# Optimization experiments

Measured on AMD Instinct MI355X. Metric: run time of the kernel, lower is better.

## Reference

```python
import jax, jax.numpy as jnp
from jax import lax
import numpy as np

NUM_TOKENS = 14
DIM = 512
B, T = 32, 512


def _lstm(xs, W_ih, W_hh, b_ih, b_hh):
    """PyTorch-semantics single-layer LSTM, batch_first. xs: [B,T,D] -> hs: [B,T,D].
    Gate order i, f, g, o; gates = x @ W_ih^T + b_ih + h @ W_hh^T + b_hh."""
    Bsz, Tlen, D = xs.shape
    # Precompute input contribution for all timesteps (one big GEMM).
    pre = jnp.einsum('btd,gd->btg', xs, W_ih) + (b_ih + b_hh)  # [B,T,4D]

    def step(carry, p):
        h, c = carry
        gates = p + h @ W_hh.T  # [B,4D]
        i, f, g, o = jnp.split(gates, 4, axis=-1)
        i = jax.nn.sigmoid(i)
        f = jax.nn.sigmoid(f)
        g = jnp.tanh(g)
        o = jax.nn.sigmoid(o)
        c = f * c + i * g
        h = o * jnp.tanh(c)
        return (h, c), h

    h0 = jnp.zeros((Bsz, D), xs.dtype)
    (_, _), hs = lax.scan(step, (h0, h0), jnp.swapaxes(pre, 0, 1))  # time-major scan
    return jnp.swapaxes(hs, 0, 1)  # [B,T,D]


def setup_inputs() -> dict:
    key = jax.random.key(0)
    ks = jax.random.split(key, 10)
    s_emb = 1.0  # nn.Embedding default init N(0,1)
    s = 1.0 / np.sqrt(DIM)  # nn.LSTM default init U(-1/sqrt(H), 1/sqrt(H))
    u = lambda k, shape: jax.random.uniform(k, shape, jnp.float32, -s, s)
    return {
        'x': jax.random.randint(ks[0], (B, T), 0, NUM_TOKENS, dtype=jnp.int32),
        'embed': jax.random.normal(ks[1], (NUM_TOKENS, DIM), jnp.float32) * s_emb,
        'W_ih_q': u(ks[2], (4 * DIM, DIM)),
        'W_hh_q': u(ks[3], (4 * DIM, DIM)),
        'b_ih_q': u(ks[4], (4 * DIM,)),
        'b_hh_q': u(ks[5], (4 * DIM,)),
        'W_ih_k': u(ks[6], (4 * DIM, DIM)),
        'W_hh_k': u(ks[7], (4 * DIM, DIM)),
        'b_ih_k': u(ks[8], (4 * DIM,)),
        'b_hh_k': u(ks[9], (4 * DIM,)),
    }


def reference(x, embed, W_ih_q, W_hh_q, b_ih_q, b_hh_q, W_ih_k, W_hh_k, b_ih_k, b_hh_k):
    e = embed[x]  # [B,T,D] embedding lookup
    q = _lstm(e, W_ih_q, W_hh_q, b_ih_q, b_hh_q)  # [B,T,D]
    k = _lstm(e, W_ih_k, W_hh_k, b_ih_k, b_hh_k)  # [B,T,D]
    A = jnp.einsum('btd,bsd->bts', q, k)  # bmm(q, k^T) -> [B,T,T]
    return A
```

## Files before the change

kernel.cpp:

```cpp
#include <hip/hip_runtime.h>
#include <hip/hip_bf16.h>


#define TB 32
#define TT 512
#define TD 512
#define NTOK 14

typedef __attribute__((ext_vector_type(8))) short short8;
typedef __attribute__((ext_vector_type(4))) float f32x4;

__device__ __forceinline__ float fsigmoid(float v) { return 1.f / (1.f + __expf(-v)); }
__device__ __forceinline__ float ftanh(float v) {
    float a = fabsf(v);
    float e = __expf(-2.f * a);
    float r = (1.f - e) / (1.f + e);
    return copysignf(r, v);
}
__device__ __forceinline__ unsigned short f2bf(float f) {
    __hip_bfloat16 h = __float2bfloat16(f);
    return __builtin_bit_cast(unsigned short, h);
}
__device__ __forceinline__ float bf2f(unsigned short u) {
    unsigned int x = ((unsigned int)u) << 16;
    return __builtin_bit_cast(float, x);
}

__device__ __forceinline__ short8 load16_coh(const unsigned short* p) {
    short8 r;
    asm volatile("global_load_dwordx4 %0, %1, off sc0 sc1" : "=v"(r) : "v"(p));
    return r;
}
__device__ __forceinline__ void store2_coh(unsigned short* p, unsigned int v) {
    asm volatile("global_store_short %0, %1, off sc0 sc1" :: "v"(p), "v"(v) : "memory");
}
__device__ __forceinline__ void store4_coh(unsigned int* p, unsigned int v) {
    asm volatile("global_store_dword %0, %1, off sc0 sc1" :: "v"(p), "v"(v) : "memory");
}
__device__ __forceinline__ unsigned int load4_coh(const unsigned int* p) {
    unsigned int r;
    asm volatile("global_load_dword %0, %1, off sc0 sc1\n\ts_waitcnt vmcnt(0)"
                 : "=v"(r) : "v"(p) : "memory");
    return r;
}

__global__ __launch_bounds__(256) void pre_tab_kernel(
    const float* __restrict__ embed,
    const float* __restrict__ Wih_q, const float* __restrict__ bih_q, const float* __restrict__ bhh_q,
    const float* __restrict__ Wih_k, const float* __restrict__ bih_k, const float* __restrict__ bhh_k,
    float* __restrict__ pre)
{
    int idx = blockIdx.x * 256 + threadIdx.x;
    int l = idx / (NTOK * 4 * TD);
    int r = idx % (NTOK * 4 * TD);
    int tok = r / (4 * TD), j = r % (4 * TD);
    const float* Wih = l ? Wih_k : Wih_q;
    float acc = l ? (bih_k[j] + bhh_k[j]) : (bih_q[j] + bhh_q[j]);
    const float4* e4 = (const float4*)(embed + (size_t)tok * TD);
    const float4* w4 = (const float4*)(Wih + (size_t)j * TD);
    for (int t2 = 0; t2 < TD / 4; ++t2) {
        float4 e = e4[t2], w = w4[t2];
        acc += e.x * w.x + e.y * w.y + e.z * w.z + e.w * w.w;
    }
    pre[idx] = acc;
}

__global__ void init_flags(unsigned int* flags) { flags[threadIdx.x] = 0; }

__global__ __launch_bounds__(256) void lstm_persist(
    const float* __restrict__ Whh_q, const float* __restrict__ Whh_k,
    const float* __restrict__ pre,
    const int* __restrict__ x,
    unsigned short* __restrict__ qh, unsigned short* __restrict__ ql,
    unsigned short* __restrict__ kh, unsigned short* __restrict__ kl,
    unsigned short* __restrict__ hbf,
    unsigned int* __restrict__ flags)
{
    __shared__ unsigned short w_lds[64][512];
    __shared__ unsigned short h_lds[16][512];
    __shared__ float          g_lds[64][17];
    __shared__ unsigned char  x_lds[16 * TT];
    __shared__ float          pre_lds[NTOK][64];

    int wg  = blockIdx.x;
    int l   = wg >> 6;
    int g   = (wg >> 5) & 1;
    int wid = wg & 31;
    int d0  = wid << 4;
    int tid = threadIdx.x;
    int lane = tid & 63;
    int rt  = tid >> 6;

    const float* Whh = l ? Whh_k : Whh_q;
    unsigned short* hi_arr = l ? kh : qh;
    unsigned short* lo_arr = l ? kl : ql;
    unsigned short* hb_l = hbf + (size_t)l * 2 * TB * TD;
    unsigned int* fl = flags + (l * 2 + g) * 32;

    {
        int r = tid >> 2;
        const float* src = Whh + (size_t)((r >> 4) * TD + d0 + (r & 15)) * TD;
#pragma unroll
        for (int i = 0; i < 16; ++i) {
            int c = (tid & 3) + 4 * i;
            float4 a = ((const float4*)src)[c * 2];
            float4 b4 = ((const float4*)src)[c * 2 + 1];
            unsigned short* dst = &w_lds[r][(c ^ (r & 7)) * 8];
            dst[0] = f2bf(a.x); dst[1] = f2bf(a.y);
            dst[2] = f2bf(a.z); dst[3] = f2bf(a.w);
            dst[4] = f2bf(b4.x); dst[5] = f2bf(b4.y);
            dst[6] = f2bf(b4.z); dst[7] = f2bf(b4.w);
        }
    }
    for (int i = tid; i < 16 * TT; i += 256)
        x_lds[i] = (unsigned char)x[(g * 16 + (i >> 9)) * TT + (i & 511)];
    for (int i = tid; i < NTOK * 64; i += 256) {
        int tok = i >> 6, j = i & 63;
        pre_lds[tok][j] = pre[((size_t)l * NTOK + tok) * (4 * TD) + (j >> 4) * TD + d0 + (j & 15)];
    }
    __syncthreads();

    int bl = tid >> 4, dd = tid & 15;
    int bg = g * 16 + bl;
    float creg = 0.f;

    {
        int tok = x_lds[bl * TT];
        float i_ = fsigmoid(pre_lds[tok][dd]);
        float f_ = fsigmoid(pre_lds[tok][16 + dd]);
        float g_ = ftanh(pre_lds[tok][32 + dd]);
        float o_ = fsigmoid(pre_lds[tok][48 + dd]);
        creg = i_ * g_;
        float h = o_ * ftanh(creg);
        unsigned short hh = f2bf(h);
        store2_coh(hb_l + (size_t)bg * TD + d0 + dd, hh);
        asm volatile("s_waitcnt vmcnt(0)" ::: "memory");
        size_t hoff = ((size_t)bg * TT) * TD + d0 + dd;
        hi_arr[hoff] = hh;
        lo_arr[hoff] = f2bf(h - bf2f(hh));
    }
    __syncthreads();
    if (tid == 0) store4_coh(fl + wid, 1u);

    for (int t = 1; t < TT; ++t) {
        {
            unsigned int need = (unsigned int)t;
            for (;;) {
                unsigned int v = load4_coh(fl + (lane & 31));
                if (__all((int)(v >= need))) break;
                __builtin_amdgcn_s_sleep(1);
            }
        }
        {
            int row = tid >> 4;
            const unsigned short* hb = hb_l + (size_t)((t - 1) & 1) * TB * TD
                                            + (size_t)(g * 16 + row) * TD;
            short8 v0 = load16_coh(hb + ((tid & 15) +  0) * 8);
            short8 v1 = load16_coh(hb + ((tid & 15) + 16) * 8);
            short8 v2 = load16_coh(hb + ((tid & 15) + 32) * 8);
            short8 v3 = load16_coh(hb + ((tid & 15) + 48) * 8);
            asm volatile("s_waitcnt vmcnt(0)" ::: "memory");
            __builtin_amdgcn_sched_barrier(0);
            *(short8*)&h_lds[row][(((tid & 15) +  0) ^ (row & 7)) * 8] = v0;
            *(short8*)&h_lds[row][(((tid & 15) + 16) ^ (row & 7)) * 8] = v1;
            *(short8*)&h_lds[row][(((tid & 15) + 32) ^ (row & 7)) * 8] = v2;
            *(short8*)&h_lds[row][(((tid & 15) + 48) ^ (row & 7)) * 8] = v3;
        }
        __syncthreads();

        {
            f32x4 acc = {0.f, 0.f, 0.f, 0.f};
            int rr = rt * 16 + (lane & 15);
            int hr = lane & 15;
#pragma unroll
            for (int kk = 0; kk < 16; ++kk) {
                int c = kk * 4 + (lane >> 4);
                short8 a  = *(const short8*)&h_lds[hr][(c ^ (hr & 7)) * 8];
                short8 bf = *(const short8*)&w_lds[rr][(c ^ (rr & 7)) * 8];
                acc = __builtin_amdgcn_mfma_f32_16x16x32_bf16(a, bf, acc, 0, 0, 0);
            }
            int gb = (lane >> 4) << 2;
#pragma unroll
            for (int r2 = 0; r2 < 4; ++r2) g_lds[rr][gb + r2] = acc[r2];
        }
        __syncthreads();

        {
            int tok = x_lds[bl * TT + t];
            float gi = g_lds[dd][bl]      + pre_lds[tok][dd];
            float gf = g_lds[16 + dd][bl] + pre_lds[tok][16 + dd];
            float gg = g_lds[32 + dd][bl] + pre_lds[tok][32 + dd];
            float go = g_lds[48 + dd][bl] + pre_lds[tok][48 + dd];
            float i_ = fsigmoid(gi), f_ = fsigmoid(gf), g2 = ftanh(gg), o_ = fsigmoid(go);
            creg = f_ * creg + i_ * g2;
            float h = o_ * ftanh(creg);
            unsigned short hh = f2bf(h);
            store2_coh(hb_l + (size_t)(t & 1) * TB * TD + (size_t)bg * TD + d0 + dd, hh);
            asm volatile("s_waitcnt vmcnt(0)" ::: "memory");
            size_t hoff = ((size_t)bg * TT + t) * TD + d0 + dd;
            hi_arr[hoff] = hh;
            lo_arr[hoff] = f2bf(h - bf2f(hh));
        }
        __syncthreads();
        if (tid == 0) store4_coh(fl + wid, (unsigned int)(t + 1));
    }
}

__global__ __launch_bounds__(256) void qk_mfma(
    const unsigned short* __restrict__ qh, const unsigned short* __restrict__ ql,
    const unsigned short* __restrict__ kh, const unsigned short* __restrict__ kl,
    float* __restrict__ A)
{
    __shared__ unsigned short qh_t[64][64];
    __shared__ unsigned short ql_t[64][64];
    __shared__ unsigned short kh_t[64][64];
    __shared__ unsigned short kl_t[64][64];

    int b  = blockIdx.y;
    int t0 = (blockIdx.x >> 3) * 64;
    int s0 = (blockIdx.x & 7) * 64;
    int tid = threadIdx.x;
    int lane = tid & 63;
    int w = tid >> 6;

    int tq = w * 16 + (lane & 15);
    f32x4 acc0 = {0,0,0,0}, acc1 = {0,0,0,0}, acc2 = {0,0,0,0}, acc3 = {0,0,0,0};

    for (int kc = 0; kc < 8; ++kc) {
        for (int i = tid; i < 512; i += 256) {
            int row = i >> 3, c = i & 7;
            size_t qoff = ((size_t)b * TT + t0 + row) * TD + kc * 64 + c * 8;
            size_t koff = ((size_t)b * TT + s0 + row) * TD + kc * 64 + c * 8;
            int d = (c ^ (row & 7)) * 8;
            *(short8*)&qh_t[row][d] = *(const short8*)(qh + qoff);
            *(short8*)&ql_t[row][d] = *(const short8*)(ql + qoff);
            *(short8*)&kh_t[row][d] = *(const short8*)(kh + koff);
            *(short8*)&kl_t[row][d] = *(const short8*)(kl + koff);
        }
        __syncthreads();
#pragma unroll
        for (int kk = 0; kk < 2; ++kk) {
            int c = kk * 4 + (lane >> 4);
            short8 ah = *(const short8*)&qh_t[tq][(c ^ (tq & 7)) * 8];
            short8 al = *(const short8*)&ql_t[tq][(c ^ (tq & 7)) * 8];
#pragma unroll
            for (int st = 0; st < 4; ++st) {
                int sr = st * 16 + (lane & 15);
                short8 bh = *(const short8*)&kh_t[sr][(c ^ (sr & 7)) * 8];
                short8 bl = *(const short8*)&kl_t[sr][(c ^ (sr & 7)) * 8];
                f32x4* acc = (st == 0) ? &acc0 : (st == 1) ? &acc1 : (st == 2) ? &acc2 : &acc3;
                *acc = __builtin_amdgcn_mfma_f32_16x16x32_bf16(ah, bh, *acc, 0, 0, 0);
                *acc = __builtin_amdgcn_mfma_f32_16x16x32_bf16(ah, bl, *acc, 0, 0, 0);
                *acc = __builtin_amdgcn_mfma_f32_16x16x32_bf16(al, bh, *acc, 0, 0, 0);
            }
        }
        __syncthreads();
    }
    int m = (lane >> 4) << 2;
    size_t base = (size_t)b * TT * TT + (size_t)(t0 + w * 16 + m) * TT + s0 + (lane & 15);
#pragma unroll
    for (int r2 = 0; r2 < 4; ++r2) {
        A[base + (size_t)r2 * TT +  0] = acc0[r2];
        A[base + (size_t)r2 * TT + 16] = acc1[r2];
        A[base + (size_t)r2 * TT + 32] = acc2[r2];
        A[base + (size_t)r2 * TT + 48] = acc3[r2];
    }
}

extern "C" void kernel_launch(void* const* d_in, const int* in_sizes, int n_in,
                              void* d_out, int out_size, void* d_ws, size_t ws_size,
                              hipStream_t stream)
{
    const int*   x      = (const int*)d_in[0];
    const float* embed  = (const float*)d_in[1];
    const float* Wih_q  = (const float*)d_in[2];
    const float* Whh_q  = (const float*)d_in[3];
    const float* bih_q  = (const float*)d_in[4];
    const float* bhh_q  = (const float*)d_in[5];
    const float* Wih_k  = (const float*)d_in[6];
    const float* Whh_k  = (const float*)d_in[7];
    const float* bih_k  = (const float*)d_in[8];
    const float* bhh_k  = (const float*)d_in[9];

    unsigned short* qh = (unsigned short*)d_ws;
    unsigned short* ql = qh + (size_t)TB * TT * TD;
    unsigned short* kh = ql + (size_t)TB * TT * TD;
    unsigned short* kl = kh + (size_t)TB * TT * TD;
    float* pre = (float*)(kl + (size_t)TB * TT * TD);
    unsigned short* hbf = (unsigned short*)(pre + 2 * NTOK * 4 * TD);
    unsigned int* flags = (unsigned int*)(hbf + 65536);

    init_flags<<<1, 128, 0, stream>>>(flags);
    pre_tab_kernel<<<224, 256, 0, stream>>>(embed, Wih_q, bih_q, bhh_q,
                                            Wih_k, bih_k, bhh_k, pre);
    lstm_persist<<<128, 256, 0, stream>>>(Whh_q, Whh_k, pre, x,
                                          qh, ql, kh, kl, hbf, flags);
    dim3 g2(64, 32);
    qk_mfma<<<g2, 256, 0, stream>>>(qh, ql, kh, kl, (float*)d_out);
}
```

Before: 1.558 ms.

## Replace per-workgroup flag barrier with timestep-tagged h values for inter-block sync

Each h element is now stored as a 32-bit word whose high half holds the bf16 value and whose low half holds the timestep tag, so consumers spin on the data itself. This removes the separate flag array, the store waitcnt and two workgroup barriers per step that existed only to publish flags. Readers first poll one word per producer, then load the whole h row and re-load any chunk whose tags don't match, unpacking the bf16 values into LDS. The cost is twice the exchange traffic per step, plus tag validation and possible re-reads. The tag is kept in 16 bits, which is enough for 512 steps.

```diff
diff --git a/kernel.cpp b/kernel.cpp
--- a/kernel.cpp
+++ b/kernel.cpp
@@ -9,6 +9,7 @@
 
 typedef __attribute__((ext_vector_type(8))) short short8;
 typedef __attribute__((ext_vector_type(4))) float f32x4;
+typedef __attribute__((ext_vector_type(4))) unsigned int u32x4;
 
 __device__ __forceinline__ float fsigmoid(float v) { return 1.f / (1.f + __expf(-v)); }
 __device__ __forceinline__ float ftanh(float v) {
@@ -26,22 +27,13 @@
     return __builtin_bit_cast(float, x);
 }
 
-__device__ __forceinline__ short8 load16_coh(const unsigned short* p) {
-    short8 r;
+__device__ __forceinline__ u32x4 load16u_coh(const unsigned int* p) {
+    u32x4 r;
     asm volatile("global_load_dwordx4 %0, %1, off sc0 sc1" : "=v"(r) : "v"(p));
     return r;
 }
-__device__ __forceinline__ void store2_coh(unsigned short* p, unsigned int v) {
-    asm volatile("global_store_short %0, %1, off sc0 sc1" :: "v"(p), "v"(v) : "memory");
-}
 __device__ __forceinline__ void store4_coh(unsigned int* p, unsigned int v) {
     asm volatile("global_store_dword %0, %1, off sc0 sc1" :: "v"(p), "v"(v) : "memory");
-}
-__device__ __forceinline__ unsigned int load4_coh(const unsigned int* p) {
-    unsigned int r;
-    asm volatile("global_load_dword %0, %1, off sc0 sc1\n\ts_waitcnt vmcnt(0)"
-                 : "=v"(r) : "v"(p) : "memory");
-    return r;
 }
 
 __global__ __launch_bounds__(256) void pre_tab_kernel(
@@ -65,7 +57,9 @@
     pre[idx] = acc;
 }
 
-__global__ void init_flags(unsigned int* flags) { flags[threadIdx.x] = 0; }
+__global__ __launch_bounds__(256) void init_hbf(unsigned int* hbf) {
+    hbf[blockIdx.x * 256 + threadIdx.x] = 0;
+}
 
 __global__ __launch_bounds__(256) void lstm_persist(
     const float* __restrict__ Whh_q, const float* __restrict__ Whh_k,
@@ -73,8 +67,7 @@
     const int* __restrict__ x,
     unsigned short* __restrict__ qh, unsigned short* __restrict__ ql,
     unsigned short* __restrict__ kh, unsigned short* __restrict__ kl,
-    unsigned short* __restrict__ hbf,
-    unsigned int* __restrict__ flags)
+    unsigned int* __restrict__ hbf)
 {
     __shared__ unsigned short w_lds[64][512];
     __shared__ unsigned short h_lds[16][512];
@@ -94,8 +87,7 @@
     const float* Whh = l ? Whh_k : Whh_q;
     unsigned short* hi_arr = l ? kh : qh;
     unsigned short* lo_arr = l ? kl : ql;
-    unsigned short* hb_l = hbf + (size_t)l * 2 * TB * TD;
-    unsigned int* fl = flags + (l * 2 + g) * 32;
+    unsigned int* hb_l = hbf + (size_t)l * 2 * TB * TD;
 
     {
         int r = tid >> 2;
@@ -133,38 +125,69 @@
         creg = i_ * g_;
         float h = o_ * ftanh(creg);
         unsigned short hh = f2bf(h);
-        store2_coh(hb_l + (size_t)bg * TD + d0 + dd, hh);
-        asm volatile("s_waitcnt vmcnt(0)" ::: "memory");
+        store4_coh(hb_l + (size_t)bg * TD + d0 + dd, ((unsigned int)hh << 16) | 1u);
         size_t hoff = ((size_t)bg * TT) * TD + d0 + dd;
         hi_arr[hoff] = hh;
         lo_arr[hoff] = f2bf(h - bf2f(hh));
     }
-    __syncthreads();
-    if (tid == 0) store4_coh(fl + wid, 1u);
 
     for (int t = 1; t < TT; ++t) {
         {
-            unsigned int need = (unsigned int)t;
+            const unsigned int e = (unsigned int)t;
+            int row = tid >> 4;
+            const unsigned int* hb = hb_l + (size_t)((t - 1) & 1) * TB * TD
+                                          + (size_t)(g * 16 + row) * TD;
+            int w2 = (tid & 15) * 2;
+            const unsigned int* s0 = hb + w2 * 16 + 15;
+            const unsigned int* s1 = hb + (w2 + 1) * 16 + 15;
             for (;;) {
-                unsigned int v = load4_coh(fl + (lane & 31));
-                if (__all((int)(v >= need))) break;
+                unsigned int v0, v1;
+                asm volatile("global_load_dword %0, %2, off sc0 sc1\n\t"
+                             "global_load_dword %1, %3, off sc0 sc1\n\t"
+                             "s_waitcnt vmcnt(0)"
+                             : "=v"(v0), "=v"(v1) : "v"(s0), "v"(s1) : "memory");
+                if (__all(((v0 & 0xffffu) >= e) && ((v1 & 0xffffu) >= e))) break;
                 __builtin_amdgcn_s_sleep(1);
             }
-        }
-        {
-            int row = tid >> 4;
-            const unsigned short* hb = hb_l + (size_t)((t - 1) & 1) * TB * TD
-                                            + (size_t)(g * 16 + row) * TD;
-            short8 v0 = load16_coh(hb + ((tid & 15) +  0) * 8);
-            short8 v1 = load16_coh(hb + ((tid & 15) + 16) * 8);
-            short8 v2 = load16_coh(hb + ((tid & 15) + 32) * 8);
-            short8 v3 = load16_coh(hb + ((tid & 15) + 48) * 8);
-            asm volatile("s_waitcnt vmcnt(0)" ::: "memory");
-            __builtin_amdgcn_sched_barrier(0);
-            *(short8*)&h_lds[row][(((tid & 15) +  0) ^ (row & 7)) * 8] = v0;
-            *(short8*)&h_lds[row][(((tid & 15) + 16) ^ (row & 7)) * 8] = v1;
-            *(short8*)&h_lds[row][(((tid & 15) + 32) ^ (row & 7)) * 8] = v2;
-            *(short8*)&h_lds[row][(((tid & 15) + 48) ^ (row & 7)) * 8] = v3;
+            u32x4 A0[4], B0[4];
+#pragma unroll
+            for (int j = 0; j < 4; ++j) {
+                int m = (tid & 15) + 16 * j;
+                A0[j] = load16u_coh(hb + m * 8);
+                B0[j] = load16u_coh(hb + m * 8 + 4);
+            }
+            unsigned int st = 0xFu;
+            for (;;) {
+                asm volatile("s_waitcnt vmcnt(0)" ::: "memory");
+                __builtin_amdgcn_sched_barrier(0);
+                unsigned int ns = 0;
+#pragma unroll
+                for (int j = 0; j < 4; ++j) if (st & (1u << j)) {
+                    unsigned int bad =
+                        ((A0[j].x ^ e) | (A0[j].y ^ e) | (A0[j].z ^ e) | (A0[j].w ^ e) |
+                         (B0[j].x ^ e) | (B0[j].y ^ e) | (B0[j].z ^ e) | (B0[j].w ^ e)) & 0xffffu;
+                    if (bad) ns |= 1u << j;
+                }
+                st = ns;
+                if (!__any(st != 0)) break;
+#pragma unroll
+                for (int j = 0; j < 4; ++j) if (st & (1u << j)) {
+                    int m = (tid & 15) + 16 * j;
+                    A0[j] = load16u_coh(hb + m * 8);
+                    B0[j] = load16u_coh(hb + m * 8 + 4);
+                }
+                __builtin_amdgcn_s_sleep(1);
+            }
+#pragma unroll
+            for (int j = 0; j < 4; ++j) {
+                int m = (tid & 15) + 16 * j;
+                u32x4 o;
+                o.x = (A0[j].x >> 16) | (A0[j].y & 0xffff0000u);
+                o.y = (A0[j].z >> 16) | (A0[j].w & 0xffff0000u);
+                o.z = (B0[j].x >> 16) | (B0[j].y & 0xffff0000u);
+                o.w = (B0[j].z >> 16) | (B0[j].w & 0xffff0000u);
+                *(u32x4*)&h_lds[row][(m ^ (row & 7)) * 8] = o;
+            }
         }
         __syncthreads();
 
@@ -195,14 +218,12 @@
             creg = f_ * creg + i_ * g2;
             float h = o_ * ftanh(creg);
             unsigned short hh = f2bf(h);
-            store2_coh(hb_l + (size_t)(t & 1) * TB * TD + (size_t)bg * TD + d0 + dd, hh);
-            asm volatile("s_waitcnt vmcnt(0)" ::: "memory");
+            store4_coh(hb_l + (size_t)(t & 1) * TB * TD + (size_t)bg * TD + d0 + dd,
+                       ((unsigned int)hh << 16) | (unsigned int)(t + 1));
             size_t hoff = ((size_t)bg * TT + t) * TD + d0 + dd;
             hi_arr[hoff] = hh;
             lo_arr[hoff] = f2bf(h - bf2f(hh));
         }
-        __syncthreads();
-        if (tid == 0) store4_coh(fl + wid, (unsigned int)(t + 1));
     }
 }
 
@@ -287,14 +308,13 @@
     unsigned short* kh = ql + (size_t)TB * TT * TD;
     unsigned short* kl = kh + (size_t)TB * TT * TD;
     float* pre = (float*)(kl + (size_t)TB * TT * TD);
-    unsigned short* hbf = (unsigned short*)(pre + 2 * NTOK * 4 * TD);
-    unsigned int* flags = (unsigned int*)(hbf + 65536);
-
-    init_flags<<<1, 128, 0, stream>>>(flags);
+    unsigned int* hbf = (unsigned int*)(pre + 2 * NTOK * 4 * TD);
+
+    init_hbf<<<256, 256, 0, stream>>>(hbf);
     pre_tab_kernel<<<224, 256, 0, stream>>>(embed, Wih_q, bih_q, bhh_q,
                                             Wih_k, bih_k, bhh_k, pre);
     lstm_persist<<<128, 256, 0, stream>>>(Whh_q, Whh_k, pre, x,
-                                          qh, ql, kh, kl, hbf, flags);
+                                          qh, ql, kh, kl, hbf);
     dim3 g2(64, 32);
     qk_mfma<<<g2, 256, 0, stream>>>(qh, ql, kh, kl, (float*)d_out);
 }
```

Result: faster. 1.484 ms (median of 2 runs) (-4.7%).
